# Kernel tuning notes

Measured on AMD Instinct MI355X. Metric: run time of the kernel, lower is better.

The kernel has to match this reference:

```python
import jax, jax.numpy as jnp
import numpy as np

N_NODES = 100000
N_EDGES = 1600000
IN_DIM, HID_DIM, OUT_DIM = 128, 128, 64


def setup_inputs() -> dict:
    key = jax.random.key(0)
    k1, k2, k3, k4 = jax.random.split(key, 4)
    x = jax.random.normal(k1, (N_NODES, IN_DIM), dtype=jnp.float32)
    edge_index = jax.random.randint(k2, (2, N_EDGES), 0, N_NODES, dtype=jnp.int64)
    # Glorot-ish init for weights, zeros for biases (as in PyG GCNConv defaults)
    W1 = jax.random.normal(k3, (IN_DIM, HID_DIM), dtype=jnp.float32) * (1.0 / np.sqrt(IN_DIM))
    b1 = jnp.zeros((HID_DIM,), dtype=jnp.float32)
    W2 = jax.random.normal(k4, (HID_DIM, OUT_DIM), dtype=jnp.float32) * (1.0 / np.sqrt(HID_DIM))
    b2 = jnp.zeros((OUT_DIM,), dtype=jnp.float32)
    return {"x": x, "edge_index": edge_index, "W1": W1, "b1": b1, "W2": W2, "b2": b2}


def _build_norm(edge_index, num_nodes):
    """Add self-loops and compute symmetric GCN normalization per edge.
    Returns (src, dst, norm) with self-loops appended."""
    loops = jnp.arange(num_nodes, dtype=edge_index.dtype)
    src = jnp.concatenate([edge_index[0], loops])
    dst = jnpp_concat = jnp.concatenate([edge_index[1], loops])
    deg = jax.ops.segment_sum(jnp.ones_like(dst, dtype=jnp.float32), dst,
                              num_segments=num_nodes)
    dinv = jax.lax.rsqrt(deg)  # deg >= 1 due to self-loops
    norm = dinv[src] * dinv[dst]  # [E + N]
    return src, dst, norm


def _gcn_conv(h, W, b, src, dst, norm, num_nodes):
    h = h @ W                                   # [N, F_out]
    msg = h[src] * norm[:, None]                # gather + scale, [E+N, F_out]
    agg = jax.ops.segment_sum(msg, dst, num_segments=num_nodes)
    return agg + b


def reference(x, edge_index, W1, b1, W2, b2):
    num_nodes = x.shape[0]
    src, dst, norm = _build_norm(edge_index, num_nodes)
    h = jax.nn.relu(_gcn_conv(x, W1, b1, src, dst, norm, num_nodes))
    return _gcn_conv(h, W2, b2, src, dst, norm, num_nodes)
```

## Files before the change

kernel.cpp:

```cpp
#include <hip/hip_runtime.h>

#define NN 100000
#define NE 1600000
#define NB 782
#define NBPAD 1024
#define CAPB 3072
#define EPB 8192
#define NROWPAD 100096
#define DPAD 136
#define OPAD 72
#define MAXE 64

typedef __attribute__((ext_vector_type(8))) short short8;
typedef __attribute__((ext_vector_type(4))) float f32x4;

__device__ __forceinline__ unsigned short bf16rn(float f) {
    unsigned u = __float_as_uint(f);
    return (unsigned short)((u + 0x7FFFu + ((u >> 16) & 1u)) >> 16);
}
__device__ __forceinline__ float4 bf2x4(uint2 g) {
    float4 r;
    r.x = __uint_as_float(g.x << 16);
    r.y = __uint_as_float(g.x & 0xFFFF0000u);
    r.z = __uint_as_float(g.y << 16);
    r.w = __uint_as_float(g.y & 0xFFFF0000u);
    return r;
}
__device__ __forceinline__ uint2 packbf4(float4 v) {
    uint2 u;
    u.x = (unsigned)bf16rn(v.x) | ((unsigned)bf16rn(v.y) << 16);
    u.y = (unsigned)bf16rn(v.z) | ((unsigned)bf16rn(v.w) << 16);
    return u;
}
__device__ __forceinline__ void acc4(float4& a, uint2 v, unsigned qb) {
    float q = __uint_as_float(qb);
    a.x = fmaf(__uint_as_float(v.x << 16), q, a.x);
    a.y = fmaf(__uint_as_float(v.x & 0xFFFF0000u), q, a.y);
    a.z = fmaf(__uint_as_float(v.y << 16), q, a.z);
    a.w = fmaf(__uint_as_float(v.y & 0xFFFF0000u), q, a.w);
}
__device__ __forceinline__ int xcd_swz(int bid, int nwg) {
    int q = nwg >> 3, r = nwg & 7;
    int x = bid & 7, j = bid >> 3;
    int base = (x < r) ? x * (q + 1) : r * (q + 1) + (x - r) * q;
    return base + j;
}

__global__ void detect_i64_k(const unsigned* __restrict__ ei, int* __restrict__ flag) {
    unsigned w = ei[2 * threadIdx.x + 1];
    unsigned long long b = __ballot(w == 0u);
    if (threadIdx.x == 0) *flag = (b == 0xFFFFFFFFFFFFFFFFull) ? 1 : 0;
}
__device__ __forceinline__ int load_node(const void* ei, int i64, long long idx) {
    return i64 ? (int)((const long long*)ei)[idx] : ((const int*)ei)[idx];
}

__global__ void cast_bf16_k(const float* __restrict__ in, ushort* __restrict__ outb,
                            long long n4) {
    long long i = (long long)blockIdx.x * 256 + threadIdx.x;
    if (i >= n4) return;
    ((uint2*)outb)[i] = packbf4(((const float4*)in)[i]);
}

__global__ void prep_wt_k(const float* __restrict__ W1, const float* __restrict__ W2,
                          ushort* __restrict__ W1t, ushort* __restrict__ W2t) {
    int i = blockIdx.x * 256 + threadIdx.x;
    if (i < 128 * 128) {
        int k = i >> 7, n = i & 127;
        W1t[n * 128 + k] = bf16rn(W1[k * 128 + n]);
    }
    if (i < 128 * 64) {
        int k = i >> 6, n = i & 63;
        W2t[n * 128 + k] = bf16rn(W2[k * 64 + n]);
    }
}

__global__ __launch_bounds__(256) void binfill_k(const void* __restrict__ ei,
                                                 const int* __restrict__ flag,
                                                 int* __restrict__ cur,
                                                 unsigned* __restrict__ bstage) {
    __shared__ unsigned binned[EPB];
    __shared__ int lcnt[NBPAD];
    __shared__ int lpos[NBPAD];
    __shared__ int gbase[NBPAD];
    __shared__ int tsum[256];
    int tid = threadIdx.x;
    long long e0 = (long long)blockIdx.x * EPB;
    int i64 = *flag;

    for (int i = tid; i < NBPAD; i += 256) lcnt[i] = 0;
    __syncthreads();

    for (int i = tid; i < EPB; i += 256) {
        long long e = e0 + i;
        if (e < NE) {
            int d = load_node(ei, i64, (long long)NE + e);
            atomicAdd(&lcnt[d >> 7], 1);
        }
    }
    __syncthreads();

    int base = tid * 4;
    int c0 = lcnt[base], c1 = lcnt[base + 1], c2 = lcnt[base + 2], c3 = lcnt[base + 3];
    int s = c0 + c1 + c2 + c3;
    tsum[tid] = s;
    __syncthreads();
    for (int off = 1; off < 256; off <<= 1) {
        int v = (tid >= off) ? tsum[tid - off] : 0;
        __syncthreads();
        tsum[tid] += v;
        __syncthreads();
    }
    int excl = tsum[tid] - s;
    int p0 = excl, p1 = excl + c0, p2 = p1 + c1, p3 = p2 + c2;
    lcnt[base] = p0; lcnt[base + 1] = p1; lcnt[base + 2] = p2; lcnt[base + 3] = p3;
    lpos[base] = p0; lpos[base + 1] = p1; lpos[base + 2] = p2; lpos[base + 3] = p3;
    if (base < NB)     gbase[base]     = c0 ? atomicAdd(&cur[base], c0) : 0;
    if (base + 1 < NB) gbase[base + 1] = c1 ? atomicAdd(&cur[base + 1], c1) : 0;
    if (base + 2 < NB) gbase[base + 2] = c2 ? atomicAdd(&cur[base + 2], c2) : 0;
    if (base + 3 < NB) gbase[base + 3] = c3 ? atomicAdd(&cur[base + 3], c3) : 0;
    __syncthreads();

    for (int i = tid; i < EPB; i += 256) {
        long long e = e0 + i;
        if (e < NE) {
            int sv = load_node(ei, i64, e);
            int d  = load_node(ei, i64, (long long)NE + e);
            int b  = d >> 7;
            int p  = atomicAdd(&lpos[b], 1);
            binned[p] = ((unsigned)(d & 127) << 17) | (unsigned)sv;
        }
    }
    __syncthreads();

    for (int b = tid; b < NB; b += 256) {
        int start = lcnt[b], endp = lpos[b];
        int gb = gbase[b];
        unsigned* dst = bstage + (long long)b * CAPB;
        for (int k = start; k < endp; k++) {
            int go = gb + (k - start);
            if (go < CAPB) dst[go] = binned[k];
        }
    }
}

__global__ __launch_bounds__(256) void regroup_k(const int* __restrict__ cur,
                                                 const unsigned* __restrict__ bstage,
                                                 int* __restrict__ cnt,
                                                 int* __restrict__ rowstart,
                                                 uint2* __restrict__ g2,
                                                 float* __restrict__ dinv) {
    __shared__ unsigned stash[CAPB];
    __shared__ int lcnt[128], lofs[128], lpos[128], sc[128];
    int tid = threadIdx.x;
    int b = blockIdx.x;

    int total = cur[b];
    if (total > CAPB) total = CAPB;
    const unsigned* seg = bstage + (long long)b * CAPB;
    for (int i = tid; i < total; i += 256) stash[i] = seg[i];
    __syncthreads();

    if (tid < 128) { lcnt[tid] = 0; lpos[tid] = 0; }
    __syncthreads();
    for (int i = tid; i < total; i += 256)
        atomicAdd(&lcnt[stash[i] >> 17], 1);
    __syncthreads();

    if (tid < 128) sc[tid] = lcnt[tid];
    __syncthreads();
    for (int off = 1; off < 128; off <<= 1) {
        int v = 0;
        if (tid < 128 && tid >= off) v = sc[tid - off];
        __syncthreads();
        if (tid < 128) sc[tid] += v;
        __syncthreads();
    }
    if (tid < 128) {
        lofs[tid] = sc[tid] - lcnt[tid];
        int node = b * 128 + tid;
        if (node < NN) {
            cnt[node] = lcnt[tid];
            rowstart[node] = b * CAPB + lofs[tid];
            dinv[node] = rsqrtf((float)(lcnt[tid] + 1));
        }
    }
    __syncthreads();

    uint2* g = g2 + (long long)b * CAPB;
    for (int i = tid; i < total; i += 256) {
        unsigned e = stash[i];
        int nl = e >> 17;
        int p = atomicAdd(&lpos[nl], 1);
        g[lofs[nl] + p] = make_uint2(e & 0x1FFFFu, (unsigned)(b * 128 + nl));
    }
}

__global__ __launch_bounds__(256) void qn_k(const int* __restrict__ cur,
                                            const float* __restrict__ dinv,
                                            uint2* __restrict__ g2) {
    int b = blockIdx.x;
    int total = cur[b];
    if (total > CAPB) total = CAPB;
    uint2* g = g2 + (long long)b * CAPB;
    for (int i = threadIdx.x; i < total; i += 256) {
        uint2 e = g[i];
        float q = dinv[e.x] * dinv[e.y];
        g[i] = make_uint2(e.x, __float_as_uint(q));
    }
}

template <int LPN, bool BIAS, bool OUTB>
__global__ __launch_bounds__(256) void pull4_k(const uint2* __restrict__ g2,
                                               const int* __restrict__ rowstart,
                                               const int* __restrict__ cnt,
                                               const float* __restrict__ dinv,
                                               const ushort* __restrict__ hb,
                                               const float* __restrict__ bias,
                                               void* __restrict__ out) {
    __shared__ uint2 ed[256 / LPN][MAXE];
    int tid = threadIdx.x;
    int nib = tid / LPN;
    int lane = tid & (LPN - 1);
    int node = xcd_swz(blockIdx.x, (int)gridDim.x) * (256 / LPN) + nib;
    if (node >= NN) return;

    const uint2* h2 = (const uint2*)hb;
    float di = dinv[node];
    float w0 = di * di;
    float4 A = make_float4(0.f, 0.f, 0.f, 0.f);
    float4 B = make_float4(0.f, 0.f, 0.f, 0.f);
    {
        float4 hv = bf2x4(h2[(unsigned)node * LPN + lane]);
        A.x = hv.x * w0; A.y = hv.y * w0; A.z = hv.z * w0; A.w = hv.w * w0;
    }

    int deg = cnt[node];
    const uint2* row = g2 + rowstart[node];
    int s = deg < MAXE ? deg : MAXE;

    for (int t = lane; t < s; t += LPN) ed[nib][t] = row[t];

    int j = 0;
    if (s >= 8) {
        uint2 v[8];
        unsigned q[8];
#pragma unroll
        for (int t = 0; t < 8; t++) {
            uint2 e = ed[nib][t];
            q[t] = e.y;
            v[t] = h2[e.x * LPN + lane];
        }
        for (; j + 16 <= s; j += 8) {
#pragma unroll
            for (int t = 0; t < 8; t++) {
                uint2 e = ed[nib][j + 8 + t];
                uint2 nv = h2[e.x * LPN + lane];
                if (t & 1) acc4(B, v[t], q[t]);
                else       acc4(A, v[t], q[t]);
                v[t] = nv; q[t] = e.y;
            }
        }
#pragma unroll
        for (int t = 0; t < 8; t++) {
            if (t & 1) acc4(B, v[t], q[t]);
            else       acc4(A, v[t], q[t]);
        }
        j += 8;
    }
    for (; j < s; j++) {
        uint2 e = ed[nib][j];
        uint2 v0 = h2[e.x * LPN + lane];
        acc4(A, v0, e.y);
    }
    for (; j < deg; j++) {
        uint2 e = row[j];
        uint2 v0 = h2[e.x * LPN + lane];
        acc4(A, v0, e.y);
    }

    float4 o;
    o.x = A.x + B.x; o.y = A.y + B.y; o.z = A.z + B.z; o.w = A.w + B.w;
    if (BIAS) {
        float4 bb = ((const float4*)bias)[lane];
        o.x += bb.x; o.y += bb.y; o.z += bb.z; o.w += bb.w;
    }
    if (OUTB)
        ((uint2*)out)[(unsigned)node * LPN + lane] = packbf4(o);
    else
        ((float4*)out)[(unsigned)node * LPN + lane] = o;
}

__global__ __launch_bounds__(256) void dgemm_mfma_k(const ushort* __restrict__ Ab,
                                                    const ushort* __restrict__ W1t,
                                                    const float* __restrict__ b1,
                                                    const ushort* __restrict__ W2t,
                                                    ushort* __restrict__ H2b) {
    __shared__ ushort Tt[4][32 * DPAD];
    __shared__ ushort Ot[4][32 * OPAD];
    int tid = threadIdx.x;
    int wv = tid >> 6, lane = tid & 63;
    int m16 = lane & 15, quad = lane >> 4;
    int row0 = blockIdx.x * 128 + wv * 32;

    short8 af[2][4];
#pragma unroll
    for (int mt = 0; mt < 2; mt++)
#pragma unroll
        for (int kc = 0; kc < 4; kc++)
            af[mt][kc] = *(const short8*)(Ab + (long long)(row0 + mt * 16 + m16) * 128
                                          + kc * 32 + quad * 8);
    f32x4 accA[2][8];
#pragma unroll
    for (int mt = 0; mt < 2; mt++)
#pragma unroll
        for (int nt = 0; nt < 8; nt++) accA[mt][nt] = (f32x4){0.f, 0.f, 0.f, 0.f};

#pragma unroll
    for (int nt = 0; nt < 8; nt++) {
#pragma unroll
        for (int kc = 0; kc < 4; kc++) {
            short8 bf = *(const short8*)(W1t + (nt * 16 + m16) * 128 + kc * 32 + quad * 8);
            accA[0][nt] = __builtin_amdgcn_mfma_f32_16x16x32_bf16(af[0][kc], bf, accA[0][nt], 0, 0, 0);
            accA[1][nt] = __builtin_amdgcn_mfma_f32_16x16x32_bf16(af[1][kc], bf, accA[1][nt], 0, 0, 0);
        }
    }

#pragma unroll
    for (int nt = 0; nt < 8; nt++) {
        float bb = b1[nt * 16 + m16];
#pragma unroll
        for (int mt = 0; mt < 2; mt++)
#pragma unroll
            for (int r = 0; r < 4; r++) {
                float v = fmaxf(accA[mt][nt][r] + bb, 0.f);
                Tt[wv][(mt * 16 + quad * 4 + r) * DPAD + nt * 16 + m16] = bf16rn(v);
            }
    }
    __syncthreads();

    f32x4 accB[2][4];
#pragma unroll
    for (int mt = 0; mt < 2; mt++)
#pragma unroll
        for (int nt = 0; nt < 4; nt++) accB[mt][nt] = (f32x4){0.f, 0.f, 0.f, 0.f};

#pragma unroll
    for (int nt = 0; nt < 4; nt++) {
#pragma unroll
        for (int kc = 0; kc < 4; kc++) {
            short8 bf = *(const short8*)(W2t + (nt * 16 + m16) * 128 + kc * 32 + quad * 8);
#pragma unroll
            for (int mt = 0; mt < 2; mt++) {
                short8 aT = *(const short8*)(&Tt[wv][(mt * 16 + m16) * DPAD + kc * 32 + quad * 8]);
                accB[mt][nt] = __builtin_amdgcn_mfma_f32_16x16x32_bf16(aT, bf, accB[mt][nt], 0, 0, 0);
            }
        }
    }

#pragma unroll
    for (int nt = 0; nt < 4; nt++)
#pragma unroll
        for (int mt = 0; mt < 2; mt++)
#pragma unroll
            for (int r = 0; r < 4; r++)
                Ot[wv][(mt * 16 + quad * 4 + r) * OPAD + nt * 16 + m16] = bf16rn(accB[mt][nt][r]);
    __syncthreads();

    uint4* H4 = (uint4*)H2b;
#pragma unroll
    for (int it = 0; it < 4; it++) {
        int idx = it * 64 + lane;
        int r = idx >> 3, c = idx & 7;
        int grow = row0 + r;
        if (grow < NN) {
            uint4 v = *(const uint4*)(&Ot[wv][r * OPAD + c * 8]);
            H4[(long long)grow * 8 + c] = v;
        }
    }
}

extern "C" void kernel_launch(void* const* d_in, const int* in_sizes, int n_in,
                              void* d_out, int out_size, void* d_ws, size_t ws_size,
                              hipStream_t stream) {
    const float* x  = (const float*)d_in[0];
    const void*  ei = d_in[1];
    const float* W1 = (const float*)d_in[2];
    const float* b1 = (const float*)d_in[3];
    const float* W2 = (const float*)d_in[4];
    const float* b2 = (const float*)d_in[5];
    float* out = (float*)d_out;
    char* ws = (char*)d_ws;

    int*      flag     = (int*)ws;
    int*      cur      = (int*)(ws + 0x1000);
    int*      cnt      = (int*)(ws + 0x10000);
    int*      rowstart = (int*)(ws + 0x80000);
    unsigned* bstage   = (unsigned*)(ws + 0x100000);
    uint2*    g2       = (uint2*)(ws + 0xB00000);
    ushort*   xb       = (ushort*)(ws + 0x1E00000);
    ushort*   aggxb    = (ushort*)(ws + 0x3700000);
    ushort*   h2b      = (ushort*)(ws + 0x5000000);
    ushort*   W1t      = (ushort*)(ws + 0x5D00000);
    ushort*   W2t      = (ushort*)(ws + 0x5D10000);
    float*    dinv     = (float*)(ws + 0x5D20000);

    hipMemsetAsync(cur, 0, NB * sizeof(int), stream);
    detect_i64_k<<<1, 64, 0, stream>>>((const unsigned*)ei, flag);
    cast_bf16_k<<<(NN * 32 + 255) / 256, 256, 0, stream>>>(x, xb, (long long)NN * 32);
    prep_wt_k<<<64, 256, 0, stream>>>(W1, W2, W1t, W2t);
    binfill_k<<<(NE + EPB - 1) / EPB, 256, 0, stream>>>(ei, flag, cur, bstage);
    regroup_k<<<NB, 256, 0, stream>>>(cur, bstage, cnt, rowstart, g2, dinv);
    qn_k<<<NB, 256, 0, stream>>>(cur, dinv, g2);

    pull4_k<32, false, true><<<(NN + 7) / 8, 256, 0, stream>>>(g2, rowstart, cnt, dinv,
                                                               xb, nullptr, aggxb);
    dgemm_mfma_k<<<NROWPAD / 128, 256, 0, stream>>>(aggxb, W1t, b1, W2t, h2b);

    pull4_k<16, true, false><<<(NN + 15) / 16, 256, 0, stream>>>(g2, rowstart, cnt, dinv,
                                                                 h2b, b2, out);
}
```

Measured before the change: 317.8 us.

## Pack edge src and quantized source dinv into one 32-bit word

Each CSR edge entry shrinks from an 8-byte (src, norm) pair to a 4-byte word holding the 17-bit source index and a 15-bit truncated mantissa of dinv[src]. The destination's dinv is multiplied in inside the pull kernels. Regroup now sorts edges in shared memory before writing them out coalesced, and binfill runs with 1024 threads, each owning one bin. This halves edge-list traffic in both aggregation passes, at the cost of reduced precision in the normalization factor, which relies on dinv lying in a fixed exponent range.

```diff
diff --git a/kernel.cpp b/kernel.cpp
--- a/kernel.cpp
+++ b/kernel.cpp
@@ -6,6 +6,7 @@
 #define NBPAD 1024
 #define CAPB 3072
 #define EPB 8192
+#define BFT 1024
 #define NROWPAD 100096
 #define DPAD 136
 #define OPAD 72
@@ -32,12 +33,14 @@
     u.y = (unsigned)bf16rn(v.z) | ((unsigned)bf16rn(v.w) << 16);
     return u;
 }
-__device__ __forceinline__ void acc4(float4& a, uint2 v, unsigned qb) {
-    float q = __uint_as_float(qb);
+__device__ __forceinline__ void acc4(float4& a, uint2 v, float q) {
     a.x = fmaf(__uint_as_float(v.x << 16), q, a.x);
     a.y = fmaf(__uint_as_float(v.x & 0xFFFF0000u), q, a.y);
     a.z = fmaf(__uint_as_float(v.y << 16), q, a.z);
     a.w = fmaf(__uint_as_float(v.y & 0xFFFF0000u), q, a.w);
+}
+__device__ __forceinline__ float decq(unsigned e) {
+    return __uint_as_float(0x38000000u | ((e & 0x7FFFu) << 12));
 }
 __device__ __forceinline__ int xcd_swz(int bid, int nwg) {
     int q = nwg >> 3, r = nwg & 7;
@@ -75,23 +78,23 @@
     }
 }
 
-__global__ __launch_bounds__(256) void binfill_k(const void* __restrict__ ei,
-                                                 const int* __restrict__ flag,
-                                                 int* __restrict__ cur,
-                                                 unsigned* __restrict__ bstage) {
+__global__ __launch_bounds__(1024) void binfill_k(const void* __restrict__ ei,
+                                                  const int* __restrict__ flag,
+                                                  int* __restrict__ cur,
+                                                  unsigned* __restrict__ bstage) {
     __shared__ unsigned binned[EPB];
     __shared__ int lcnt[NBPAD];
     __shared__ int lpos[NBPAD];
     __shared__ int gbase[NBPAD];
-    __shared__ int tsum[256];
+    __shared__ int tsum[NBPAD];
     int tid = threadIdx.x;
     long long e0 = (long long)blockIdx.x * EPB;
     int i64 = *flag;
 
-    for (int i = tid; i < NBPAD; i += 256) lcnt[i] = 0;
-    __syncthreads();
-
-    for (int i = tid; i < EPB; i += 256) {
+    lcnt[tid] = 0;
+    __syncthreads();
+
+    for (int i = tid; i < EPB; i += BFT) {
         long long e = e0 + i;
         if (e < NE) {
             int d = load_node(ei, i64, (long long)NE + e);
@@ -100,28 +103,22 @@
     }
     __syncthreads();
 
-    int base = tid * 4;
-    int c0 = lcnt[base], c1 = lcnt[base + 1], c2 = lcnt[base + 2], c3 = lcnt[base + 3];
-    int s = c0 + c1 + c2 + c3;
-    tsum[tid] = s;
-    __syncthreads();
-    for (int off = 1; off < 256; off <<= 1) {
+    int c = lcnt[tid];
+    tsum[tid] = c;
+    __syncthreads();
+    for (int off = 1; off < NBPAD; off <<= 1) {
         int v = (tid >= off) ? tsum[tid - off] : 0;
         __syncthreads();
         tsum[tid] += v;
         __syncthreads();
     }
-    int excl = tsum[tid] - s;
-    int p0 = excl, p1 = excl + c0, p2 = p1 + c1, p3 = p2 + c2;
-    lcnt[base] = p0; lcnt[base + 1] = p1; lcnt[base + 2] = p2; lcnt[base + 3] = p3;
-    lpos[base] = p0; lpos[base + 1] = p1; lpos[base + 2] = p2; lpos[base + 3] = p3;
-    if (base < NB)     gbase[base]     = c0 ? atomicAdd(&cur[base], c0) : 0;
-    if (base + 1 < NB) gbase[base + 1] = c1 ? atomicAdd(&cur[base + 1], c1) : 0;
-    if (base + 2 < NB) gbase[base + 2] = c2 ? atomicAdd(&cur[base + 2], c2) : 0;
-    if (base + 3 < NB) gbase[base + 3] = c3 ? atomicAdd(&cur[base + 3], c3) : 0;
-    __syncthreads();
-
-    for (int i = tid; i < EPB; i += 256) {
+    int excl = tsum[tid] - c;
+    lcnt[tid] = excl;
+    lpos[tid] = excl;
+    if (tid < NB) gbase[tid] = c ? atomicAdd(&cur[tid], c) : 0;
+    __syncthreads();
+
+    for (int i = tid; i < EPB; i += BFT) {
         long long e = e0 + i;
         if (e < NE) {
             int sv = load_node(ei, i64, e);
@@ -133,10 +130,10 @@
     }
     __syncthreads();
 
-    for (int b = tid; b < NB; b += 256) {
-        int start = lcnt[b], endp = lpos[b];
-        int gb = gbase[b];
-        unsigned* dst = bstage + (long long)b * CAPB;
+    if (tid < NB) {
+        int start = lcnt[tid], endp = lpos[tid];
+        int gb = gbase[tid];
+        unsigned* dst = bstage + (long long)tid * CAPB;
         for (int k = start; k < endp; k++) {
             int go = gb + (k - start);
             if (go < CAPB) dst[go] = binned[k];
@@ -148,9 +145,10 @@
                                                  const unsigned* __restrict__ bstage,
                                                  int* __restrict__ cnt,
                                                  int* __restrict__ rowstart,
-                                                 uint2* __restrict__ g2,
+                                                 unsigned* __restrict__ grouped,
                                                  float* __restrict__ dinv) {
     __shared__ unsigned stash[CAPB];
+    __shared__ unsigned srt[CAPB];
     __shared__ int lcnt[128], lofs[128], lpos[128], sc[128];
     int tid = threadIdx.x;
     int b = blockIdx.x;
@@ -187,38 +185,41 @@
     }
     __syncthreads();
 
-    uint2* g = g2 + (long long)b * CAPB;
     for (int i = tid; i < total; i += 256) {
         unsigned e = stash[i];
         int nl = e >> 17;
         int p = atomicAdd(&lpos[nl], 1);
-        g[lofs[nl] + p] = make_uint2(e & 0x1FFFFu, (unsigned)(b * 128 + nl));
-    }
-}
-
-__global__ __launch_bounds__(256) void qn_k(const int* __restrict__ cur,
-                                            const float* __restrict__ dinv,
-                                            uint2* __restrict__ g2) {
+        srt[lofs[nl] + p] = e;
+    }
+    __syncthreads();
+
+    unsigned* g = grouped + (long long)b * CAPB;
+    for (int i = tid; i < total; i += 256) g[i] = srt[i] & 0x1FFFFu;
+}
+
+__global__ __launch_bounds__(256) void qn2_k(const int* __restrict__ cur,
+                                             const float* __restrict__ dinv,
+                                             unsigned* __restrict__ grouped) {
     int b = blockIdx.x;
     int total = cur[b];
     if (total > CAPB) total = CAPB;
-    uint2* g = g2 + (long long)b * CAPB;
+    unsigned* g = grouped + (long long)b * CAPB;
     for (int i = threadIdx.x; i < total; i += 256) {
-        uint2 e = g[i];
-        float q = dinv[e.x] * dinv[e.y];
-        g[i] = make_uint2(e.x, __float_as_uint(q));
+        unsigned s = g[i];
+        unsigned bits = __float_as_uint(dinv[s]);
+        g[i] = (s << 15) | ((bits >> 12) & 0x7FFFu);
     }
 }
 
 template <int LPN, bool BIAS, bool OUTB>
-__global__ __launch_bounds__(256) void pull4_k(const uint2* __restrict__ g2,
+__global__ __launch_bounds__(256) void pull6_k(const unsigned* __restrict__ grouped,
                                                const int* __restrict__ rowstart,
                                                const int* __restrict__ cnt,
                                                const float* __restrict__ dinv,
                                                const ushort* __restrict__ hb,
                                                const float* __restrict__ bias,
                                                void* __restrict__ out) {
-    __shared__ uint2 ed[256 / LPN][MAXE];
+    __shared__ unsigned ed[256 / LPN][MAXE];
     int tid = threadIdx.x;
     int nib = tid / LPN;
     int lane = tid & (LPN - 1);
@@ -236,7 +237,7 @@
     }
 
     int deg = cnt[node];
-    const uint2* row = g2 + rowstart[node];
+    const unsigned* row = grouped + rowstart[node];
     int s = deg < MAXE ? deg : MAXE;
 
     for (int t = lane; t < s; t += LPN) ed[nib][t] = row[t];
@@ -244,21 +245,21 @@
     int j = 0;
     if (s >= 8) {
         uint2 v[8];
-        unsigned q[8];
+        float q[8];
 #pragma unroll
         for (int t = 0; t < 8; t++) {
-            uint2 e = ed[nib][t];
-            q[t] = e.y;
-            v[t] = h2[e.x * LPN + lane];
+            unsigned e = ed[nib][t];
+            q[t] = decq(e) * di;
+            v[t] = h2[(e >> 15) * LPN + lane];
         }
         for (; j + 16 <= s; j += 8) {
 #pragma unroll
             for (int t = 0; t < 8; t++) {
-                uint2 e = ed[nib][j + 8 + t];
-                uint2 nv = h2[e.x * LPN + lane];
+                unsigned e = ed[nib][j + 8 + t];
+                uint2 nv = h2[(e >> 15) * LPN + lane];
                 if (t & 1) acc4(B, v[t], q[t]);
                 else       acc4(A, v[t], q[t]);
-                v[t] = nv; q[t] = e.y;
+                v[t] = nv; q[t] = decq(e) * di;
             }
         }
 #pragma unroll
@@ -269,14 +270,14 @@
         j += 8;
     }
     for (; j < s; j++) {
-        uint2 e = ed[nib][j];
-        uint2 v0 = h2[e.x * LPN + lane];
-        acc4(A, v0, e.y);
+        unsigned e = ed[nib][j];
+        uint2 v0 = h2[(e >> 15) * LPN + lane];
+        acc4(A, v0, decq(e) * di);
     }
     for (; j < deg; j++) {
-        uint2 e = row[j];
-        uint2 v0 = h2[e.x * LPN + lane];
-        acc4(A, v0, e.y);
+        unsigned e = row[j];
+        uint2 v0 = h2[(e >> 15) * LPN + lane];
+        acc4(A, v0, decq(e) * di);
     }
 
     float4 o;
@@ -397,26 +398,26 @@
     int*      cnt      = (int*)(ws + 0x10000);
     int*      rowstart = (int*)(ws + 0x80000);
     unsigned* bstage   = (unsigned*)(ws + 0x100000);
-    uint2*    g2       = (uint2*)(ws + 0xB00000);
-    ushort*   xb       = (ushort*)(ws + 0x1E00000);
-    ushort*   aggxb    = (ushort*)(ws + 0x3700000);
-    ushort*   h2b      = (ushort*)(ws + 0x5000000);
-    ushort*   W1t      = (ushort*)(ws + 0x5D00000);
-    ushort*   W2t      = (ushort*)(ws + 0x5D10000);
-    float*    dinv     = (float*)(ws + 0x5D20000);
+    unsigned* grouped  = (unsigned*)(ws + 0xB00000);
+    ushort*   xb       = (ushort*)(ws + 0x1500000);
+    ushort*   aggxb    = (ushort*)(ws + 0x2F00000);
+    ushort*   h2b      = (ushort*)(ws + 0x4800000);
+    ushort*   W1t      = (ushort*)(ws + 0x5500000);
+    ushort*   W2t      = (ushort*)(ws + 0x5510000);
+    float*    dinv     = (float*)(ws + 0x5520000);
 
     hipMemsetAsync(cur, 0, NB * sizeof(int), stream);
     detect_i64_k<<<1, 64, 0, stream>>>((const unsigned*)ei, flag);
     cast_bf16_k<<<(NN * 32 + 255) / 256, 256, 0, stream>>>(x, xb, (long long)NN * 32);
     prep_wt_k<<<64, 256, 0, stream>>>(W1, W2, W1t, W2t);
-    binfill_k<<<(NE + EPB - 1) / EPB, 256, 0, stream>>>(ei, flag, cur, bstage);
-    regroup_k<<<NB, 256, 0, stream>>>(cur, bstage, cnt, rowstart, g2, dinv);
-    qn_k<<<NB, 256, 0, stream>>>(cur, dinv, g2);
-
-    pull4_k<32, false, true><<<(NN + 7) / 8, 256, 0, stream>>>(g2, rowstart, cnt, dinv,
+    binfill_k<<<(NE + EPB - 1) / EPB, BFT, 0, stream>>>(ei, flag, cur, bstage);
+    regroup_k<<<NB, 256, 0, stream>>>(cur, bstage, cnt, rowstart, grouped, dinv);
+    qn2_k<<<NB, 256, 0, stream>>>(cur, dinv, grouped);
+
+    pull6_k<32, false, true><<<(NN + 7) / 8, 256, 0, stream>>>(grouped, rowstart, cnt, dinv,
                                                                xb, nullptr, aggxb);
     dgemm_mfma_k<<<NROWPAD / 128, 256, 0, stream>>>(aggxb, W1t, b1, W2t, h2b);
 
-    pull4_k<16, true, false><<<(NN + 15) / 16, 256, 0, stream>>>(g2, rowstart, cnt, dinv,
+    pull6_k<16, true, false><<<(NN + 15) / 16, 256, 0, stream>>>(grouped, rowstart, cnt, dinv,
                                                                  h2b, b2, out);
 }
```

Result: faster. 278.1 us (-12.5%).
